# Kernel optimization log

Measured on AMD Instinct MI355X. Metric: run time of the kernel, lower is better.

Reference implementation:

```python
import jax, jax.numpy as jnp
import numpy as np

# dims per module source / chosen globals
B, LB = 4, 28            # new frames, buffered frames; M = B+LB = L = 32
DK, DV = 256, 32         # Dk=256 hardcoded; Dv = 4*len_of_lookup+4 with len_of_lookup=7
HS, WS = 64, 64          # H//8, W//8 with H=W=512
LMAX = 32                # memory cap L
TRAIN_SZ = 1000          # log base train_sz
ALPHA = 0.5              # blend coefficient (original inits 0, which zeroes the branch)
# log(L*h*w + h*w, train_sz) / sqrt(Dk)
SCALE = float(np.log(LMAX * HS * WS + HS * WS) / np.log(TRAIN_SZ) / np.sqrt(DK))


def _xavier(key, fan_in, fan_out):
    lim = np.sqrt(6.0 / (fan_in + fan_out))
    return jax.random.uniform(key, (fan_in, fan_out), jnp.float32, -lim, lim)


def setup_inputs() -> dict:
    key = jax.random.key(0)
    ks = jax.random.split(key, 7)
    return {
        "fc": jax.random.normal(ks[0], (B, DK, HS, WS), jnp.float32),
        "fm": jax.random.normal(ks[1], (B, DV, HS, WS), jnp.float32),
        "key_buffer": jax.random.normal(ks[2], (LB, DK, HS, WS), jnp.float32),
        "value_buffer": jax.random.normal(ks[3], (LB, DV, HS, WS), jnp.float32),
        "Q": _xavier(ks[4], DK, DK),
        "K": _xavier(ks[5], DK, DK),
        "V": _xavier(ks[6], DV, DV),
    }


def reference(fc, fm, key_buffer, value_buffer, Q, K, V):
    # matmul = einsum('ijkl,jm->imkl'): per-pixel channel mixing
    q = jnp.einsum('bdhw,de->behw', fc, Q)                      # [B,Dk,h,w]
    k = jnp.concatenate([jnp.einsum('bdhw,de->behw', fc, K), key_buffer], axis=0)    # [M,Dk,h,w]
    v = jnp.concatenate([jnp.einsum('bdhw,de->behw', fm, V), value_buffer], axis=0)  # [M,Dv,h,w]
    # current_batch (=1) < L, so no slicing of k/v on this step
    scores = SCALE * jnp.einsum('bdhw,mdhw->bmhw', q, k)        # [B,M,h,w]
    attn = jax.nn.softmax(scores, axis=-1)                      # NOTE: softmax over width axis, as in source (dim=-1)
    ctx = jnp.einsum('bmhw,mdhw->bdhw', attn, v)                # [B,Dv,h,w]
    return fm + ALPHA * ctx
```

## Files before the change

kernel.cpp:

```cpp
#include <hip/hip_runtime.h>
#include <hip/hip_bf16.h>
#include <cmath>

#define NB 4
#define NM 32
#define DKc 256
#define DVc 32
#define NP 4096

using bf16x8 = __attribute__((ext_vector_type(8))) short;
using f32x4  = __attribute__((ext_vector_type(4))) float;

__device__ __forceinline__ unsigned short f2bf(float f) {
    union { float f; unsigned u; } x; x.f = f;
    unsigned r = 0x7FFFu + ((x.u >> 16) & 1u);
    return (unsigned short)((x.u + r) >> 16);
}
__device__ __forceinline__ float bf2f(unsigned short s) { union { unsigned u; float f; } x; x.u = ((unsigned)s) << 16; return x.f; }

__global__ __launch_bounds__(256) void k_prep(
    const float* __restrict__ fc, unsigned short* __restrict__ fcT,
    const float* __restrict__ Q, unsigned short* __restrict__ WTq,
    const float* __restrict__ K, unsigned short* __restrict__ WTk,
    const float* __restrict__ fm, const float* __restrict__ V, float* __restrict__ vproj) {
    int x = blockIdx.x;
    int t = threadIdx.x;
    if (x < 1056) {
        __shared__ float tile[64][65];
        const float* s; unsigned short* d; int R, C, r0, c0;
        if (x < 1024) {
            int bb = x >> 8, rest = x & 255;
            R = 256; C = 4096;
            r0 = (rest >> 6) * 64; c0 = (rest & 63) * 64;
            s = fc + (long)bb * 256 * 4096; d = fcT + (long)bb * 256 * 4096;
        } else {
            int i = x - 1024;
            int mat = i >> 4, idx = i & 15;
            R = 256; C = 256;
            r0 = (idx >> 2) * 64; c0 = (idx & 3) * 64;
            s = mat ? K : Q; d = mat ? WTk : WTq;
        }
        #pragma unroll
        for (int j = 0; j < 16; ++j) {
            int i = t + 256 * j;
            int r = i >> 6, c = i & 63;
            tile[r][c] = s[(long)(r0 + r) * C + c0 + c];
        }
        __syncthreads();
        #pragma unroll
        for (int j = 0; j < 8; ++j) {
            int i = t + 256 * j;
            int row = i >> 5;
            int pr = i & 31;
            float f0 = tile[2 * pr][row];
            float f1 = tile[2 * pr + 1][row];
            unsigned pack = (unsigned)f2bf(f0) | ((unsigned)f2bf(f1) << 16);
            reinterpret_cast<unsigned*>(d)[(((long)(c0 + row) * R + r0) >> 1) + pr] = pack;
        }
    } else {
        __shared__ float Vl[32][32];
        __shared__ float fml[32][256];
        int i = x - 1056;
        int b = i >> 4, p0 = (i & 15) * 256;
        #pragma unroll
        for (int j = 0; j < 4; ++j) { int ii = t + 256 * j; Vl[ii >> 5][ii & 31] = V[ii]; }
        for (int j = 0; j < 32; ++j) {
            int ii = t + 256 * j;
            int dd = ii >> 8, c = ii & 255;
            fml[dd][c] = fm[((long)b * DVc + dd) * NP + p0 + c];
        }
        __syncthreads();
        float acc[32];
        #pragma unroll
        for (int e = 0; e < 32; ++e) acc[e] = 0.f;
        for (int dd = 0; dd < 32; ++dd) {
            float fv = fml[dd][t];
            #pragma unroll
            for (int e = 0; e < 32; ++e) acc[e] += fv * Vl[dd][e];
        }
        #pragma unroll
        for (int e = 0; e < 32; ++e) vproj[((long)b * DVc + e) * NP + p0 + t] = acc[e];
    }
}

__global__ __launch_bounds__(256) void k_proj(
    const unsigned short* __restrict__ WTq, const unsigned short* __restrict__ WTk,
    const unsigned short* __restrict__ fcT,
    unsigned short* __restrict__ qT, float* __restrict__ kproj) {
    int t = threadIdx.x;
    int wave = t >> 6, lane = t & 63;
    int y = blockIdx.y;
    int b = y & 3, mat = y >> 2;
    int p0 = blockIdx.x * 64;
    int ln = lane & 15, quad = lane >> 4;
    const unsigned short* WT = mat ? WTk : WTq;
    int e0w = wave * 64;
    const unsigned short* bbase = fcT + ((long)b * NP + p0 + ln) * DKc + quad * 8;
    f32x4 acc[4][4] = {};
    for (int kk = 0; kk < DKc; kk += 32) {
        bf16x8 a[4], bb[4];
        #pragma unroll
        for (int i = 0; i < 4; ++i)
            a[i] = *reinterpret_cast<const bf16x8*>(WT + (long)(e0w + i * 16 + ln) * DKc + quad * 8 + kk);
        #pragma unroll
        for (int j = 0; j < 4; ++j)
            bb[j] = *reinterpret_cast<const bf16x8*>(bbase + (long)j * 16 * DKc + kk);
        #pragma unroll
        for (int i = 0; i < 4; ++i)
            #pragma unroll
            for (int j = 0; j < 4; ++j)
                acc[i][j] = __builtin_amdgcn_mfma_f32_16x16x32_bf16(a[i], bb[j], acc[i][j], 0, 0, 0);
    }
    if (mat == 0) {
        #pragma unroll
        for (int i = 0; i < 4; ++i)
            #pragma unroll
            for (int j = 0; j < 4; ++j)
                #pragma unroll
                for (int r = 0; r < 4; ++r) {
                    int e = e0w + i * 16 + quad * 4 + r, p = p0 + j * 16 + ln;
                    qT[((long)b * NP + p) * DKc + e] = f2bf(acc[i][j][r]);
                }
    } else {
        #pragma unroll
        for (int i = 0; i < 4; ++i)
            #pragma unroll
            for (int j = 0; j < 4; ++j)
                #pragma unroll
                for (int r = 0; r < 4; ++r) {
                    int e = e0w + i * 16 + quad * 4 + r, p = p0 + j * 16 + ln;
                    kproj[((long)b * DKc + e) * NP + p] = acc[i][j][r];
                }
    }
}

__global__ __launch_bounds__(512, 2) void k_fused(
    const unsigned short* __restrict__ qT, const float* __restrict__ kproj,
    const float* __restrict__ kbuf, const float* __restrict__ vproj,
    const float* __restrict__ vbuf, const float* __restrict__ fm,
    float* __restrict__ out, float scale) {
    __shared__ float smemf[256 * 68];
    __shared__ float sc[32][68];
    float (*LDSq)[68] = reinterpret_cast<float (*)[68]>(smemf);
    float (*red)[32][68] = reinterpret_cast<float (*)[32][68]>(smemf);
    int t = threadIdx.x;
    int b = blockIdx.x >> 6, hrow = blockIdx.x & 63;
    int p0h = hrow * 64;

    {
        const unsigned short* qtile = qT + ((long)b * NP + p0h) * DKc;
        int ec = t >> 6, p = t & 63;
        #pragma unroll
        for (int s = 0; s < 4; ++s) {
            int e0 = ec * 32 + s * 8;
            bf16x8 v8 = *reinterpret_cast<const bf16x8*>(qtile + (long)p * DKc + e0);
            #pragma unroll
            for (int i = 0; i < 8; ++i) LDSq[e0 + i][p] = bf2f((unsigned short)v8[i]);
        }
    }
    __syncthreads();

    int wq = t & 15, eg = t >> 4;
    f32x4 q4[8];
    #pragma unroll
    for (int j = 0; j < 8; ++j)
        q4[j] = *reinterpret_cast<const f32x4*>(&LDSq[eg * 8 + j][wq * 4]);
    __syncthreads();

    f32x4 acc[NM];
    #pragma unroll
    for (int m = 0; m < NM; ++m) acc[m] = (f32x4){0.f, 0.f, 0.f, 0.f};
    #pragma unroll
    for (int m = 0; m < NM; ++m) {
        const float* kp = (m < 4 ? kproj + (long)m * DKc * NP : kbuf + (long)(m - 4) * DKc * NP)
                          + (long)(eg * 8) * NP + p0h + wq * 4;
        #pragma unroll
        for (int j = 0; j < 8; ++j) {
            f32x4 kv = *reinterpret_cast<const f32x4*>(kp + (long)j * NP);
            acc[m] += q4[j] * kv;
        }
    }
    #pragma unroll
    for (int m = 0; m < NM; ++m)
        #pragma unroll
        for (int c = 0; c < 4; ++c) {
            float v = acc[m][c];
            v += __shfl_xor(v, 16);
            v += __shfl_xor(v, 32);
            acc[m][c] = v;
        }
    int wave = t >> 6, lane = t & 63;
    if (lane < 16) {
        #pragma unroll
        for (int m = 0; m < NM; ++m)
            *reinterpret_cast<f32x4*>(&red[wave][m][lane * 4]) = acc[m];
    }
    __syncthreads();
    {
        int m = t >> 4, w0 = (t & 15) * 4;
        f32x4 s = (f32x4){0.f, 0.f, 0.f, 0.f};
        #pragma unroll
        for (int v = 0; v < 8; ++v) s += *reinterpret_cast<const f32x4*>(&red[v][m][w0]);
        f32x4 sv = s * scale;
        *reinterpret_cast<f32x4*>(&sc[m][w0]) = sv;
    }
    __syncthreads();
    {
        #pragma unroll
        for (int r = 0; r < 4; ++r) {
            int m = wave * 4 + r;
            float x = sc[m][lane];
            float mx = x;
            #pragma unroll
            for (int d = 1; d < 64; d <<= 1) mx = fmaxf(mx, __shfl_xor(mx, d));
            float e = __expf(x - mx);
            float sum = e;
            #pragma unroll
            for (int d = 1; d < 64; d <<= 1) sum += __shfl_xor(sum, d);
            sc[m][lane] = e / sum;
        }
    }
    __syncthreads();
    {
        int w = t & 63, dg = t >> 6;
        f32x4 c = (f32x4){0.f, 0.f, 0.f, 0.f};
        #pragma unroll
        for (int m = 0; m < NM; ++m) {
            float a = sc[m][w];
            const float* vp = (m < 4 ? vproj + (long)m * DVc * NP : vbuf + (long)(m - 4) * DVc * NP)
                              + (long)(dg * 4) * NP + p0h + w;
            #pragma unroll
            for (int i = 0; i < 4; ++i) c[i] += a * vp[(long)i * NP];
        }
        #pragma unroll
        for (int i = 0; i < 4; ++i) {
            long gi = ((long)b * DVc + dg * 4 + i) * NP + p0h + w;
            out[gi] = fm[gi] + 0.5f * c[i];
        }
    }
}

extern "C" void kernel_launch(void* const* d_in, const int* in_sizes, int n_in,
                              void* d_out, int out_size, void* d_ws, size_t ws_size,
                              hipStream_t stream) {
    const float* fc = (const float*)d_in[0];
    const float* fm = (const float*)d_in[1];
    const float* kb = (const float*)d_in[2];
    const float* vb = (const float*)d_in[3];
    const float* Q  = (const float*)d_in[4];
    const float* K  = (const float*)d_in[5];
    const float* V  = (const float*)d_in[6];
    float* out = (float*)d_out;
    char* ws = (char*)d_ws;
    unsigned short* fcT   = (unsigned short*)(ws);
    unsigned short* WTq   = (unsigned short*)(ws + 8388608);
    unsigned short* WTk   = (unsigned short*)(ws + 8519680);
    unsigned short* qT    = (unsigned short*)(ws + 8650752);
    float*          kproj = (float*)(ws + 17039360);
    float*          vproj = (float*)(ws + 33816576);
    float scale = (float)(log(135168.0) / log(1000.0) / 16.0);

    hipLaunchKernelGGL(k_prep, dim3(1120), dim3(256), 0, stream,
                       fc, fcT, Q, WTq, K, WTk, fm, V, vproj);
    hipLaunchKernelGGL(k_proj, dim3(64, 8), dim3(256), 0, stream,
                       WTq, WTk, fcT, qT, kproj);
    hipLaunchKernelGGL(k_fused, dim3(256), dim3(512), 0, stream,
                       qT, kproj, kb, vproj, vb, fm, out, scale);
}
```

Before: 257.0 us.

## Store q in fp32 channel-major and widen fused attention block to 1024 threads

The projection kernel now writes q as fp32 in the same channel-major layout as k, so the fused kernel loads q directly into registers instead of transposing bf16 through LDS. The fused kernel uses 1024 threads per block, with each thread covering 4 channels instead of 8. Score accumulation is split into two chunks of 16 memory frames to limit register use, with a padded LDS reduction, and the value stage computes 2 channels per thread. This adds fp32 q traffic (twice the bf16 bytes) and an extra round of block barriers in exchange for more threads hiding the latency of the large key_buffer reads.

Result: slower. 263.0 us (+2.3%).

```diff
diff --git a/kernel.cpp b/kernel.cpp
--- a/kernel.cpp
+++ b/kernel.cpp
@@ -16,7 +16,6 @@
     unsigned r = 0x7FFFu + ((x.u >> 16) & 1u);
     return (unsigned short)((x.u + r) >> 16);
 }
-__device__ __forceinline__ float bf2f(unsigned short s) { union { unsigned u; float f; } x; x.u = ((unsigned)s) << 16; return x.f; }
 
 __global__ __launch_bounds__(256) void k_prep(
     const float* __restrict__ fc, unsigned short* __restrict__ fcT,
@@ -86,7 +85,7 @@
 __global__ __launch_bounds__(256) void k_proj(
     const unsigned short* __restrict__ WTq, const unsigned short* __restrict__ WTk,
     const unsigned short* __restrict__ fcT,
-    unsigned short* __restrict__ qT, float* __restrict__ kproj) {
+    float* __restrict__ qproj, float* __restrict__ kproj) {
     int t = threadIdx.x;
     int wave = t >> 6, lane = t & 63;
     int y = blockIdx.y;
@@ -94,6 +93,7 @@
     int p0 = blockIdx.x * 64;
     int ln = lane & 15, quad = lane >> 4;
     const unsigned short* WT = mat ? WTk : WTq;
+    float* dst = mat ? kproj : qproj;
     int e0w = wave * 64;
     const unsigned short* bbase = fcT + ((long)b * NP + p0 + ln) * DKc + quad * 8;
     f32x4 acc[4][4] = {};
@@ -111,132 +111,106 @@
             for (int j = 0; j < 4; ++j)
                 acc[i][j] = __builtin_amdgcn_mfma_f32_16x16x32_bf16(a[i], bb[j], acc[i][j], 0, 0, 0);
     }
-    if (mat == 0) {
-        #pragma unroll
-        for (int i = 0; i < 4; ++i)
-            #pragma unroll
-            for (int j = 0; j < 4; ++j)
-                #pragma unroll
-                for (int r = 0; r < 4; ++r) {
-                    int e = e0w + i * 16 + quad * 4 + r, p = p0 + j * 16 + ln;
-                    qT[((long)b * NP + p) * DKc + e] = f2bf(acc[i][j][r]);
-                }
-    } else {
-        #pragma unroll
-        for (int i = 0; i < 4; ++i)
-            #pragma unroll
-            for (int j = 0; j < 4; ++j)
-                #pragma unroll
-                for (int r = 0; r < 4; ++r) {
-                    int e = e0w + i * 16 + quad * 4 + r, p = p0 + j * 16 + ln;
-                    kproj[((long)b * DKc + e) * NP + p] = acc[i][j][r];
-                }
-    }
-}
-
-__global__ __launch_bounds__(512, 2) void k_fused(
-    const unsigned short* __restrict__ qT, const float* __restrict__ kproj,
+    #pragma unroll
+    for (int i = 0; i < 4; ++i)
+        #pragma unroll
+        for (int j = 0; j < 4; ++j)
+            #pragma unroll
+            for (int r = 0; r < 4; ++r) {
+                int e = e0w + i * 16 + quad * 4 + r, p = p0 + j * 16 + ln;
+                dst[((long)b * DKc + e) * NP + p] = acc[i][j][r];
+            }
+}
+
+__global__ __launch_bounds__(1024, 4) void k_fused(
+    const float* __restrict__ qproj, const float* __restrict__ kproj,
     const float* __restrict__ kbuf, const float* __restrict__ vproj,
     const float* __restrict__ vbuf, const float* __restrict__ fm,
     float* __restrict__ out, float scale) {
-    __shared__ float smemf[256 * 68];
+    __shared__ float red[16 * 1099];
     __shared__ float sc[32][68];
-    float (*LDSq)[68] = reinterpret_cast<float (*)[68]>(smemf);
-    float (*red)[32][68] = reinterpret_cast<float (*)[32][68]>(smemf);
     int t = threadIdx.x;
     int b = blockIdx.x >> 6, hrow = blockIdx.x & 63;
     int p0h = hrow * 64;
-
-    {
-        const unsigned short* qtile = qT + ((long)b * NP + p0h) * DKc;
-        int ec = t >> 6, p = t & 63;
-        #pragma unroll
-        for (int s = 0; s < 4; ++s) {
-            int e0 = ec * 32 + s * 8;
-            bf16x8 v8 = *reinterpret_cast<const bf16x8*>(qtile + (long)p * DKc + e0);
-            #pragma unroll
-            for (int i = 0; i < 8; ++i) LDSq[e0 + i][p] = bf2f((unsigned short)v8[i]);
-        }
-    }
-    __syncthreads();
-
-    int wq = t & 15, eg = t >> 4;
-    f32x4 q4[8];
-    #pragma unroll
-    for (int j = 0; j < 8; ++j)
-        q4[j] = *reinterpret_cast<const f32x4*>(&LDSq[eg * 8 + j][wq * 4]);
-    __syncthreads();
-
-    f32x4 acc[NM];
-    #pragma unroll
-    for (int m = 0; m < NM; ++m) acc[m] = (f32x4){0.f, 0.f, 0.f, 0.f};
-    #pragma unroll
-    for (int m = 0; m < NM; ++m) {
-        const float* kp = (m < 4 ? kproj + (long)m * DKc * NP : kbuf + (long)(m - 4) * DKc * NP)
-                          + (long)(eg * 8) * NP + p0h + wq * 4;
-        #pragma unroll
-        for (int j = 0; j < 8; ++j) {
-            f32x4 kv = *reinterpret_cast<const f32x4*>(kp + (long)j * NP);
-            acc[m] += q4[j] * kv;
-        }
-    }
-    #pragma unroll
-    for (int m = 0; m < NM; ++m)
-        #pragma unroll
-        for (int c = 0; c < 4; ++c) {
-            float v = acc[m][c];
-            v += __shfl_xor(v, 16);
-            v += __shfl_xor(v, 32);
-            acc[m][c] = v;
-        }
     int wave = t >> 6, lane = t & 63;
-    if (lane < 16) {
-        #pragma unroll
-        for (int m = 0; m < NM; ++m)
-            *reinterpret_cast<f32x4*>(&red[wave][m][lane * 4]) = acc[m];
+    int wq = lane & 15, egw = lane >> 4;
+    int e0 = wave * 16 + egw * 4;
+    int w0 = wq * 4;
+
+    f32x4 qv[4];
+    const float* qp = qproj + ((long)b * DKc + e0) * NP + p0h + w0;
+    #pragma unroll
+    for (int j = 0; j < 4; ++j) qv[j] = *reinterpret_cast<const f32x4*>(qp + (long)j * NP);
+
+    #pragma unroll
+    for (int mc = 0; mc < 2; ++mc) {
+        f32x4 acc[16];
+        #pragma unroll
+        for (int mi = 0; mi < 16; ++mi) acc[mi] = (f32x4){0.f, 0.f, 0.f, 0.f};
+        #pragma unroll
+        for (int mi = 0; mi < 16; ++mi) {
+            int m = mc * 16 + mi;
+            const float* kp = (m < 4 ? kproj + (long)m * DKc * NP : kbuf + (long)(m - 4) * DKc * NP)
+                              + (long)e0 * NP + p0h + w0;
+            #pragma unroll
+            for (int j = 0; j < 4; ++j) {
+                f32x4 kv = *reinterpret_cast<const f32x4*>(kp + (long)j * NP);
+                acc[mi] += qv[j] * kv;
+            }
+        }
+        #pragma unroll
+        for (int mi = 0; mi < 16; ++mi)
+            #pragma unroll
+            for (int c = 0; c < 4; ++c) {
+                float v = acc[mi][c];
+                v += __shfl_xor(v, 16);
+                v += __shfl_xor(v, 32);
+                acc[mi][c] = v;
+            }
+        if (lane < 16) {
+            #pragma unroll
+            for (int mi = 0; mi < 16; ++mi)
+                *reinterpret_cast<f32x4*>(&red[wave * 1099 + mi * 69 + lane * 4]) = acc[mi];
+        }
+        __syncthreads();
+        {
+            int mr = t >> 6, w = t & 63;
+            float s = 0.f;
+            #pragma unroll
+            for (int v = 0; v < 16; ++v) s += red[v * 1099 + mr * 69 + w];
+            sc[mc * 16 + mr][w] = s * scale;
+        }
+        __syncthreads();
+    }
+    #pragma unroll
+    for (int r = 0; r < 2; ++r) {
+        int m = wave * 2 + r;
+        float x = sc[m][lane];
+        float mx = x;
+        #pragma unroll
+        for (int d = 1; d < 64; d <<= 1) mx = fmaxf(mx, __shfl_xor(mx, d));
+        float e = __expf(x - mx);
+        float sum = e;
+        #pragma unroll
+        for (int d = 1; d < 64; d <<= 1) sum += __shfl_xor(sum, d);
+        sc[m][lane] = e / sum;
     }
     __syncthreads();
     {
-        int m = t >> 4, w0 = (t & 15) * 4;
-        f32x4 s = (f32x4){0.f, 0.f, 0.f, 0.f};
-        #pragma unroll
-        for (int v = 0; v < 8; ++v) s += *reinterpret_cast<const f32x4*>(&red[v][m][w0]);
-        f32x4 sv = s * scale;
-        *reinterpret_cast<f32x4*>(&sc[m][w0]) = sv;
-    }
-    __syncthreads();
-    {
-        #pragma unroll
-        for (int r = 0; r < 4; ++r) {
-            int m = wave * 4 + r;
-            float x = sc[m][lane];
-            float mx = x;
-            #pragma unroll
-            for (int d = 1; d < 64; d <<= 1) mx = fmaxf(mx, __shfl_xor(mx, d));
-            float e = __expf(x - mx);
-            float sum = e;
-            #pragma unroll
-            for (int d = 1; d < 64; d <<= 1) sum += __shfl_xor(sum, d);
-            sc[m][lane] = e / sum;
-        }
-    }
-    __syncthreads();
-    {
-        int w = t & 63, dg = t >> 6;
-        f32x4 c = (f32x4){0.f, 0.f, 0.f, 0.f};
+        int dg = t >> 6, w = t & 63;
+        float c0 = 0.f, c1 = 0.f;
         #pragma unroll
         for (int m = 0; m < NM; ++m) {
             float a = sc[m][w];
             const float* vp = (m < 4 ? vproj + (long)m * DVc * NP : vbuf + (long)(m - 4) * DVc * NP)
-                              + (long)(dg * 4) * NP + p0h + w;
-            #pragma unroll
-            for (int i = 0; i < 4; ++i) c[i] += a * vp[(long)i * NP];
-        }
-        #pragma unroll
-        for (int i = 0; i < 4; ++i) {
-            long gi = ((long)b * DVc + dg * 4 + i) * NP + p0h + w;
-            out[gi] = fm[gi] + 0.5f * c[i];
-        }
+                              + (long)(dg * 2) * NP + p0h + w;
+            c0 += a * vp[0];
+            c1 += a * vp[NP];
+        }
+        long gi0 = ((long)b * DVc + dg * 2) * NP + p0h + w;
+        long gi1 = gi0 + NP;
+        out[gi0] = fm[gi0] + 0.5f * c0;
+        out[gi1] = fm[gi1] + 0.5f * c1;
     }
 }
 
@@ -255,15 +229,15 @@
     unsigned short* fcT   = (unsigned short*)(ws);
     unsigned short* WTq   = (unsigned short*)(ws + 8388608);
     unsigned short* WTk   = (unsigned short*)(ws + 8519680);
-    unsigned short* qT    = (unsigned short*)(ws + 8650752);
-    float*          kproj = (float*)(ws + 17039360);
-    float*          vproj = (float*)(ws + 33816576);
+    float*          qproj = (float*)(ws + 8650752);
+    float*          kproj = (float*)(ws + 25427968);
+    float*          vproj = (float*)(ws + 42205184);
     float scale = (float)(log(135168.0) / log(1000.0) / 16.0);
 
     hipLaunchKernelGGL(k_prep, dim3(1120), dim3(256), 0, stream,
                        fc, fcT, Q, WTq, K, WTk, fm, V, vproj);
     hipLaunchKernelGGL(k_proj, dim3(64, 8), dim3(256), 0, stream,
-                       WTq, WTk, fcT, qT, kproj);
-    hipLaunchKernelGGL(k_fused, dim3(256), dim3(512), 0, stream,
-                       qT, kproj, kb, vproj, vb, fm, out, scale);
-}
+                       WTq, WTk, fcT, qproj, kproj);
+    hipLaunchKernelGGL(k_fused, dim3(256), dim3(1024), 0, stream,
+                       qproj, kproj, kb, vproj, vb, fm, out, scale);
+}
```
